# Kernel optimization log

Hardware: AMD Instinct MI355X
Metric: run time of the kernel (lower is better)

Reference implementation:

```python
import jax, jax.numpy as jnp
import numpy as np

B, S, D = 4, 2048, 1024
H, DK, DV = 16, 64, 64
NEG = -1e10


def setup_inputs() -> dict:
    key = jax.random.key(0)
    ks = jax.random.split(key, 7)
    queries = jax.random.normal(ks[0], (B, S, D), dtype=jnp.float32)
    keys = jax.random.normal(ks[1], (B, S, D), dtype=jnp.float32)
    values = jax.random.normal(ks[2], (B, S, D), dtype=jnp.float32)
    mask = jnp.ones((B, S, S), dtype=jnp.int32)
    # per-head Linear weights, torch layout [out, in]; stacked over heads
    Wq = jax.random.normal(ks[3], (H, DK, D), dtype=jnp.float32) / np.sqrt(D)
    Wk = jax.random.normal(ks[4], (H, DK, D), dtype=jnp.float32) / np.sqrt(D)
    Wv = jax.random.normal(ks[5], (H, DV, D), dtype=jnp.float32) / np.sqrt(D)
    Wo = jax.random.normal(ks[6], (D, H * DV), dtype=jnp.float32) / np.sqrt(H * DV)
    return {"queries": queries, "keys": keys, "values": values, "mask": mask,
            "Wq": Wq, "Wk": Wk, "Wv": Wv, "Wo": Wo}


def reference(queries, keys, values, mask, Wq, Wk, Wv, Wo):
    # per-head projections, vectorized over heads: y = x @ W_h^T
    q = jnp.einsum('bsd,hkd->bhsk', queries, Wq)   # [B,H,S,DK]
    k = jnp.einsum('btd,hkd->bhtk', keys, Wk)      # [B,H,S,DK]
    v = jnp.einsum('btd,hvd->bhtv', values, Wv)    # [B,H,S,DV]
    scores = jnp.einsum('bhsk,bhtk->bhst', q, k) / jnp.sqrt(jnp.asarray(DK, q.dtype))
    scores = jnp.where(mask[:, None, :, :] == 0, jnp.asarray(NEG, q.dtype), scores)
    attn = jax.nn.softmax(scores, axis=-1)
    out = jnp.einsum('bhst,bhtv->bhsv', attn, v)   # [B,H,S,DV]
    # torch.cat over heads on last dim == head-major concat per position
    out = out.transpose(0, 2, 1, 3).reshape(B, S, H * DV)
    return out @ Wo.T
```

## Files before the change

kernel.cpp:

```cpp
#include <hip/hip_runtime.h>
#include <stdint.h>

typedef __attribute__((ext_vector_type(4))) float f32x4;
typedef __attribute__((ext_vector_type(8))) __bf16 bf16x8;
typedef __attribute__((ext_vector_type(4))) __bf16 bf16x4;
typedef __attribute__((ext_vector_type(4))) short s16x4;
typedef __attribute__((ext_vector_type(2))) uint32_t u32x2;

#define MFMA16(a, b, c) __builtin_amdgcn_mfma_f32_16x16x32_bf16(a, b, c, 0, 0, 0)
#define MFMA16K16(a, b, c) __builtin_amdgcn_mfma_f32_16x16x16bf16_1k(a, b, c, 0, 0, 0)

#define B_ 4
#define S_ 2048
#define D_ 1024
#define H_ 16
#define NEG_ -1e10f
#define QSCALE 0.180336880f

__device__ __forceinline__ float ex2(float x) { return __builtin_amdgcn_exp2f(x); }

__device__ __forceinline__ void glds16(const void* gsrc, void* ldst) {
  __builtin_amdgcn_global_load_lds(
      (__attribute__((address_space(1))) void*)(gsrc),
      (__attribute__((address_space(3))) void*)(ldst),
      16, 0, 0);
}

__device__ __forceinline__ uint32_t pack_bf16(float a, float b) {
  uint32_t ua = (uint32_t)__builtin_bit_cast(unsigned short, (__bf16)a);
  uint32_t ub = (uint32_t)__builtin_bit_cast(unsigned short, (__bf16)b);
  return ua | (ub << 16);
}

__global__ __launch_bounds__(256) void prep(
    const float* __restrict__ xq, const float* __restrict__ xk, const float* __restrict__ xv,
    const float* __restrict__ wq, const float* __restrict__ wk, const float* __restrict__ wv,
    const float* __restrict__ wo,
    __bf16* __restrict__ oxq, __bf16* __restrict__ oxk, __bf16* __restrict__ oxv,
    __bf16* __restrict__ owq, __bf16* __restrict__ owk, __bf16* __restrict__ owv,
    __bf16* __restrict__ owo,
    const int* __restrict__ mask, uint32_t* __restrict__ bits, int* __restrict__ flags) {
  int bid = blockIdx.x, tid = threadIdx.x;
  __shared__ int andred;
  if (bid < 24576) {
    int z = bid >> 13, xb = bid & 8191;
    const float* in = (z == 0) ? xq : (z == 1) ? xk : xv;
    __bf16* out = (z == 0) ? oxq : (z == 1) ? oxk : oxv;
    int i = (xb * 256 + tid) * 4;
    float4 v = *(const float4*)(in + i);
    bf16x4 o;
    o.x = (__bf16)v.x; o.y = (__bf16)v.y; o.z = (__bf16)v.z; o.w = (__bf16)v.w;
    *(bf16x4*)(out + i) = o;
  } else if (bid < 28672) {
    int m = bid - 24576;
    int z = m >> 10, wb = m & 1023;
    const float* in = (z == 0) ? wq : (z == 1) ? wk : (z == 2) ? wv : wo;
    __bf16* out = (z == 0) ? owq : (z == 1) ? owk : (z == 2) ? owv : owo;
    int i = (wb * 256 + tid) * 4;
    float4 v = *(const float4*)(in + i);
    bf16x4 o;
    o.x = (__bf16)v.x; o.y = (__bf16)v.y; o.z = (__bf16)v.z; o.w = (__bf16)v.w;
    *(bf16x4*)(out + i) = o;
  } else {
    int m = bid - 28672;
    int tt = m & 15, st = (m >> 4) & 15, b = m >> 8;
    int w = tid >> 6, lane = tid & 63;
    if (tid == 0) andred = 1;
    __syncthreads();
    unsigned long long all1 = ~0ull;
    for (int rr = 0; rr < 32; rr++) {
      int srow = st * 128 + w * 32 + rr;
      #pragma unroll
      for (int half = 0; half < 2; half++) {
        int c = tt * 128 + half * 64 + lane;
        int mm = mask[((size_t)b * S_ + srow) * S_ + c];
        unsigned long long bal = __ballot(mm != 0);
        all1 &= bal;
        if (lane == 0) {
          uint32_t* dst = &bits[((size_t)b * S_ + srow) * 64 + tt * 4 + half * 2];
          dst[0] = (uint32_t)bal;
          dst[1] = (uint32_t)(bal >> 32);
        }
      }
    }
    if (all1 != ~0ull) atomicAnd(&andred, 0);
    __syncthreads();
    if (tid == 0) flags[(b * 16 + st) * 16 + tt] = andred;
  }
}

template <int MODE>
__global__ __launch_bounds__(256, 3) void gemm_bt(
    const __bf16* __restrict__ A0, const __bf16* __restrict__ A1, const __bf16* __restrict__ A2,
    const __bf16* __restrict__ W0, const __bf16* __restrict__ W1, const __bf16* __restrict__ W2,
    void* O0, void* O1, void* O2) {
  const int K = 1024;
  const __bf16* PA; const __bf16* PB; void* O;
  int pa_t, pb_t;
  if (MODE == 0) {
    if (blockIdx.z == 0)      { PA = W0; PB = A0; O = O0; pa_t = blockIdx.x; pb_t = blockIdx.y; }
    else if (blockIdx.z == 1) { PA = W1; PB = A1; O = O1; pa_t = blockIdx.x; pb_t = blockIdx.y; }
    else                      { PA = A2; PB = W2; O = O2; pa_t = blockIdx.y; pb_t = blockIdx.x; }
  } else { PA = W0; PB = A0; O = O0; pa_t = blockIdx.x; pb_t = blockIdx.y; }

  __shared__ __align__(16) __bf16 As[128 * 64];
  __shared__ __align__(16) __bf16 Bs[128 * 64];
  int tid = threadIdx.x, lane = tid & 63, w = tid >> 6;
  int wm = w >> 1, wn = w & 1;
  int g = lane >> 4, l15 = lane & 15;
  f32x4 acc[4][4] = {};
  const __bf16* Ablk = PA + (size_t)(pa_t * 128) * K;
  const __bf16* Bblk = PB + (size_t)(pb_t * 128) * K;

  for (int kt = 0; kt < K; kt += 64) {
    __syncthreads();
    #pragma unroll
    for (int r = 0; r < 4; r++) {
      int C = r * 256 + tid;
      int row = C >> 3, c = C & 7;
      int c0 = c ^ (row & 7);
      glds16(Ablk + (size_t)row * K + kt + c0 * 8, (char*)As + C * 16);
      glds16(Bblk + (size_t)row * K + kt + c0 * 8, (char*)Bs + C * 16);
    }
    __syncthreads();
    #pragma unroll
    for (int kkq = 0; kkq < 2; kkq++) {
      bf16x8 af[4], bfr[4];
      #pragma unroll
      for (int i = 0; i < 4; i++) {
        int row = wm * 64 + i * 16 + l15;
        int ch = (kkq * 4 + g) ^ (row & 7);
        af[i] = *(const bf16x8*)((const char*)As + row * 128 + ch * 16);
      }
      #pragma unroll
      for (int j = 0; j < 4; j++) {
        int row = wn * 64 + j * 16 + l15;
        int ch = (kkq * 4 + g) ^ (row & 7);
        bfr[j] = *(const bf16x8*)((const char*)Bs + row * 128 + ch * 16);
      }
      #pragma unroll
      for (int i = 0; i < 4; i++)
        #pragma unroll
        for (int j = 0; j < 4; j++)
          acc[i][j] = MFMA16(af[i], bfr[j], acc[i][j]);
    }
  }

  if (MODE == 1) {
    #pragma unroll
    for (int i = 0; i < 4; i++)
      #pragma unroll
      for (int j = 0; j < 4; j++) {
        int n0 = pa_t * 128 + wm * 64 + i * 16 + g * 4;
        int m = pb_t * 128 + wn * 64 + j * 16 + l15;
        *(f32x4*)((float*)O + (size_t)m * 1024 + n0) = acc[i][j];
      }
  } else if (blockIdx.z == 2) {
    #pragma unroll
    for (int i = 0; i < 4; i++)
      #pragma unroll
      for (int j = 0; j < 4; j++) {
        int s0 = pa_t * 128 + wm * 64 + i * 16 + g * 4;
        int dvg = pb_t * 128 + wn * 64 + j * 16 + l15;
        int b = s0 >> 11, s = s0 & 2047;
        int h = dvg >> 6, dv = dvg & 63;
        bf16x4 o;
        #pragma unroll
        for (int r = 0; r < 4; r++) o[r] = (__bf16)acc[i][j][r];
        *(bf16x4*)((__bf16*)O + (((size_t)b * 16 + h) * 64 + dv) * 2048 + s) = o;
      }
  } else {
    float scale = (blockIdx.z == 0) ? QSCALE : 1.0f;
    #pragma unroll
    for (int i = 0; i < 4; i++)
      #pragma unroll
      for (int j = 0; j < 4; j++) {
        int dkg = pa_t * 128 + wm * 64 + i * 16 + g * 4;
        int sg = pb_t * 128 + wn * 64 + j * 16 + l15;
        int h = dkg >> 6, dk = dkg & 63;
        int b = sg >> 11, s = sg & 2047;
        bf16x4 o;
        #pragma unroll
        for (int r = 0; r < 4; r++) o[r] = (__bf16)(acc[i][j][r] * scale);
        *(bf16x4*)((__bf16*)O + (((size_t)b * 16 + h) * 2048 + s) * 64 + dk) = o;
      }
  }
}

__global__ __launch_bounds__(256, 2) void attn(
    const __bf16* __restrict__ qp, const __bf16* __restrict__ kp,
    const __bf16* __restrict__ vt_, __bf16* __restrict__ aout,
    const uint32_t* __restrict__ bits, const int* __restrict__ flags) {
  int qt = blockIdx.x, bh = blockIdx.y, b = bh >> 4, h = bh & 15;
  int tid = threadIdx.x, lane = tid & 63, w = tid >> 6;
  int g = lane >> 4, l15 = lane & 15;

  __shared__ __align__(16) char smem[65536];

  const __bf16* Qg = qp + ((size_t)bh * S_ + qt * 128) * 64;
  const __bf16* Kg = kp + (size_t)bh * S_ * 64;
  const __bf16* Vg = vt_ + (size_t)bh * 64 * S_;

  #pragma unroll
  for (int r = 0; r < 4; r++) {
    int C = r * 256 + tid;
    int row = C >> 3, c = C & 7, c0 = c ^ (row & 7);
    glds16(Qg + row * 64 + c0 * 8, smem + C * 16);
  }
  __syncthreads();
  bf16x8 qf[2][2];
  #pragma unroll
  for (int i = 0; i < 2; i++)
    #pragma unroll
    for (int kkq = 0; kkq < 2; kkq++) {
      int row = w * 32 + i * 16 + l15;
      int ch = (kkq * 4 + g) ^ (row & 7);
      qf[i][kkq] = *(const bf16x8*)(smem + row * 128 + ch * 16);
    }
  __syncthreads();

  auto stageKV = [&](int kt2, int p) {
    char* Kl = smem + p * 32768;
    char* Vl = Kl + 16384;
    const __bf16* Ks = Kg + (size_t)kt2 * 128 * 64;
    #pragma unroll
    for (int r = 0; r < 4; r++) {
      int C = r * 256 + tid;
      int row = C >> 3, c = C & 7, c0 = c ^ (row & 7);
      glds16(Ks + row * 64 + c0 * 8, Kl + C * 16);
    }
    #pragma unroll
    for (int r = 0; r < 4; r++) {
      int C = r * 256 + tid;
      int row = C >> 4, c = C & 15;
      int c0 = (c & 8) | ((c & 7) ^ (row & 7));
      glds16(Vg + (size_t)row * S_ + kt2 * 128 + c0 * 8, Vl + C * 16);
    }
  };

  f32x4 oacc[4][2] = {};
  f32x4 sumacc[2] = {};
  float mst[2] = {-INFINITY, -INFINITY};
  const f32x4 zero4 = {0.f, 0.f, 0.f, 0.f};
  const s16x4 ones = {(short)0x3F80, (short)0x3F80, (short)0x3F80, (short)0x3F80};

  stageKV(0, 0);
  asm volatile("s_waitcnt vmcnt(0)" ::: "memory");
  __builtin_amdgcn_s_barrier();
  __builtin_amdgcn_sched_barrier(0);

  for (int kt = 0; kt < 16; kt++) {
    int cur = kt & 1;
    if (kt + 1 < 16) stageKV(kt + 1, cur ^ 1);
    __builtin_amdgcn_sched_barrier(0);

    const char* Klds = smem + cur * 32768;
    const char* Vlds = Klds + 16384;
    int fl = flags[(b * 16 + qt) * 16 + kt];

    f32x4 sacc[2][8];
    __builtin_amdgcn_s_setprio(1);
    #pragma unroll
    for (int jt = 0; jt < 8; jt++) {
      int row = jt * 16 + l15;
      bf16x8 kf0 = *(const bf16x8*)(Klds + row * 128 + (g ^ (row & 7)) * 16);
      bf16x8 kf1 = *(const bf16x8*)(Klds + row * 128 + ((4 + g) ^ (row & 7)) * 16);
      sacc[0][jt] = MFMA16(kf0, qf[0][0], zero4);
      sacc[0][jt] = MFMA16(kf1, qf[0][1], sacc[0][jt]);
      sacc[1][jt] = MFMA16(kf0, qf[1][0], zero4);
      sacc[1][jt] = MFMA16(kf1, qf[1][1], sacc[1][jt]);
    }
    __builtin_amdgcn_s_setprio(0);

    if (!fl) {
      #pragma unroll
      for (int i = 0; i < 2; i++) {
        int srow = qt * 128 + w * 32 + i * 16 + l15;
        const uint32_t* bw = &bits[((size_t)b * S_ + srow) * 64 + kt * 4];
        uint32_t mw[4] = {bw[0], bw[1], bw[2], bw[3]};
        #pragma unroll
        for (int jt = 0; jt < 8; jt++)
          #pragma unroll
          for (int r = 0; r < 4; r++) {
            int bitpos = (jt & 1) * 16 + g * 4 + r;
            if (!((mw[jt >> 1] >> bitpos) & 1)) sacc[i][jt][r] = NEG_;
          }
      }
    }

    float mx[2];
    #pragma unroll
    for (int i = 0; i < 2; i++) {
      float m = -INFINITY;
      #pragma unroll
      for (int jt = 0; jt < 8; jt++) {
        float a = fmaxf(fmaxf(sacc[i][jt][0], sacc[i][jt][1]),
                        fmaxf(sacc[i][jt][2], sacc[i][jt][3]));
        m = fmaxf(m, a);
      }
      m = fmaxf(m, __shfl_xor(m, 16));
      m = fmaxf(m, __shfl_xor(m, 32));
      mx[i] = m;
    }

    bool need = (mx[0] > mst[0] + 8.f) || (mx[1] > mst[1] + 8.f);
    if (__any(need)) {
      float alpha[2];
      #pragma unroll
      for (int i = 0; i < 2; i++) {
        float mnew = fmaxf(mst[i], mx[i]);
        alpha[i] = ex2(mst[i] - mnew);
        mst[i] = mnew;
      }
      #pragma unroll
      for (int vt = 0; vt < 4; vt++)
        #pragma unroll
        for (int i = 0; i < 2; i++)
          #pragma unroll
          for (int r = 0; r < 4; r++) oacc[vt][i][r] *= alpha[i];
      #pragma unroll
      for (int i = 0; i < 2; i++)
        #pragma unroll
        for (int r = 0; r < 4; r++) sumacc[i][r] *= alpha[i];
    }

    #pragma unroll
    for (int jt = 0; jt < 8; jt++) {
      s16x4 pf[2];
      #pragma unroll
      for (int i = 0; i < 2; i++) {
        float p0 = ex2(sacc[i][jt][0] - mst[i]);
        float p1 = ex2(sacc[i][jt][1] - mst[i]);
        float p2 = ex2(sacc[i][jt][2] - mst[i]);
        float p3 = ex2(sacc[i][jt][3] - mst[i]);
        u32x2 t;
        t.x = pack_bf16(p0, p1);
        t.y = pack_bf16(p2, p3);
        pf[i] = __builtin_bit_cast(s16x4, t);
      }
      int ch = jt * 2 + (g >> 1);
      __builtin_amdgcn_s_setprio(1);
      #pragma unroll
      for (int vt = 0; vt < 4; vt++) {
        int row = vt * 16 + l15;
        int chs = (ch & 8) | ((ch & 7) ^ (row & 7));
        s16x4 vv = *(const s16x4*)(Vlds + row * 256 + chs * 16 + (g & 1) * 8);
        oacc[vt][0] = MFMA16K16(vv, pf[0], oacc[vt][0]);
        oacc[vt][1] = MFMA16K16(vv, pf[1], oacc[vt][1]);
      }
      sumacc[0] = MFMA16K16(ones, pf[0], sumacc[0]);
      sumacc[1] = MFMA16K16(ones, pf[1], sumacc[1]);
      __builtin_amdgcn_s_setprio(0);
    }

    asm volatile("s_waitcnt vmcnt(0)" ::: "memory");
    __builtin_amdgcn_s_barrier();
    __builtin_amdgcn_sched_barrier(0);
  }

  #pragma unroll
  for (int i = 0; i < 2; i++) {
    float inv = 1.0f / sumacc[i][0];
    int srow = qt * 128 + w * 32 + i * 16 + l15;
    #pragma unroll
    for (int vt = 0; vt < 4; vt++) {
      bf16x4 o;
      #pragma unroll
      for (int r = 0; r < 4; r++) o[r] = (__bf16)(oacc[vt][i][r] * inv);
      *(bf16x4*)(aout + ((size_t)b * S_ + srow) * 1024 + h * 64 + vt * 16 + g * 4) = o;
    }
  }
}

extern "C" void kernel_launch(void* const* d_in, const int* in_sizes, int n_in,
                              void* d_out, int out_size, void* d_ws, size_t ws_size,
                              hipStream_t stream) {
  const float* queries = (const float*)d_in[0];
  const float* keys    = (const float*)d_in[1];
  const float* values  = (const float*)d_in[2];
  const int*   mask    = (const int*)d_in[3];
  const float* Wq      = (const float*)d_in[4];
  const float* Wk      = (const float*)d_in[5];
  const float* Wv      = (const float*)d_in[6];
  const float* Wo      = (const float*)d_in[7];

  char* ws = (char*)d_ws;
  __bf16* Xq  = (__bf16*)(ws + 0);
  __bf16* Xk  = (__bf16*)(ws + 16777216);
  __bf16* Xv  = (__bf16*)(ws + 33554432);
  __bf16* Wqb = (__bf16*)(ws + 50331648);
  __bf16* Wkb = (__bf16*)(ws + 52428800);
  __bf16* Wvb = (__bf16*)(ws + 54525952);
  __bf16* Wob = (__bf16*)(ws + 56623104);
  __bf16* qp  = (__bf16*)(ws + 58720256);
  __bf16* kp  = (__bf16*)(ws + 75497472);
  __bf16* vT  = (__bf16*)(ws + 92274688);
  uint32_t* bits = (uint32_t*)(ws + 109051904);
  int* flags     = (int*)(ws + 111149056);
  __bf16* aout = Xq;

  prep<<<29696, 256, 0, stream>>>(queries, keys, values, Wq, Wk, Wv, Wo,
                                  Xq, Xk, Xv, Wqb, Wkb, Wvb, Wob,
                                  mask, bits, flags);

  gemm_bt<0><<<dim3(8, 64, 3), 256, 0, stream>>>(Xq, Xk, Xv, Wqb, Wkb, Wvb,
                                                 (void*)qp, (void*)kp, (void*)vT);

  attn<<<dim3(16, 64), 256, 0, stream>>>(qp, kp, vT, aout, bits, flags);

  gemm_bt<1><<<dim3(8, 64, 1), 256, 0, stream>>>(aout, nullptr, nullptr, Wob, nullptr, nullptr,
                                                 (void*)d_out, nullptr, nullptr);
}
```

Baseline: 424.9 us.

## Swizzle block order and stage V through registers with half-swap to cut LDS conflicts

Remaps block indices in both the projection GEMM and the attention kernel so consecutive workgroups are spread across tiles, aiming for better cache locality across XCDs. The V tile is now loaded into registers and written to LDS with a row-dependent 8-byte half swap instead of a direct global-to-LDS copy. The matching read offset is XORed so the 8-byte V fragment reads hit fewer LDS bank conflicts. This adds register pressure and an explicit LDS write plus lgkmcnt wait at the end of each iteration, which can reduce the overlap of loads with compute.

```diff
diff --git a/kernel.cpp b/kernel.cpp
--- a/kernel.cpp
+++ b/kernel.cpp
@@ -95,13 +95,17 @@
     const __bf16* __restrict__ W0, const __bf16* __restrict__ W1, const __bf16* __restrict__ W2,
     void* O0, void* O1, void* O2) {
   const int K = 1024;
+  int lin = blockIdx.y * 8 + blockIdx.x;
+  int swz = (lin & 7) * 64 + (lin >> 3);
+  int bx = swz & 7, by = swz >> 3;
+
   const __bf16* PA; const __bf16* PB; void* O;
   int pa_t, pb_t;
   if (MODE == 0) {
-    if (blockIdx.z == 0)      { PA = W0; PB = A0; O = O0; pa_t = blockIdx.x; pb_t = blockIdx.y; }
-    else if (blockIdx.z == 1) { PA = W1; PB = A1; O = O1; pa_t = blockIdx.x; pb_t = blockIdx.y; }
-    else                      { PA = A2; PB = W2; O = O2; pa_t = blockIdx.y; pb_t = blockIdx.x; }
-  } else { PA = W0; PB = A0; O = O0; pa_t = blockIdx.x; pb_t = blockIdx.y; }
+    if (blockIdx.z == 0)      { PA = W0; PB = A0; O = O0; pa_t = bx; pb_t = by; }
+    else if (blockIdx.z == 1) { PA = W1; PB = A1; O = O1; pa_t = bx; pb_t = by; }
+    else                      { PA = A2; PB = W2; O = O2; pa_t = by; pb_t = bx; }
+  } else { PA = W0; PB = A0; O = O0; pa_t = bx; pb_t = by; }
 
   __shared__ __align__(16) __bf16 As[128 * 64];
   __shared__ __align__(16) __bf16 Bs[128 * 64];
@@ -191,9 +195,13 @@
     const __bf16* __restrict__ qp, const __bf16* __restrict__ kp,
     const __bf16* __restrict__ vt_, __bf16* __restrict__ aout,
     const uint32_t* __restrict__ bits, const int* __restrict__ flags) {
-  int qt = blockIdx.x, bh = blockIdx.y, b = bh >> 4, h = bh & 15;
+  int lin = blockIdx.y * 16 + blockIdx.x;
+  int swz = (lin & 7) * 128 + (lin >> 3);
+  int qt = swz & 15, bh = swz >> 4;
+  int b = bh >> 4, h = bh & 15;
   int tid = threadIdx.x, lane = tid & 63, w = tid >> 6;
   int g = lane >> 4, l15 = lane & 15;
+  int hs0 = ((g & 1) ^ ((l15 >> 3) & 1)) * 8;
 
   __shared__ __align__(16) char smem[65536];
 
@@ -219,22 +227,37 @@
     }
   __syncthreads();
 
-  auto stageKV = [&](int kt2, int p) {
+  auto stageK = [&](int kt2, int p) {
     char* Kl = smem + p * 32768;
-    char* Vl = Kl + 16384;
     const __bf16* Ks = Kg + (size_t)kt2 * 128 * 64;
     #pragma unroll
     for (int r = 0; r < 4; r++) {
       int C = r * 256 + tid;
       int row = C >> 3, c = C & 7, c0 = c ^ (row & 7);
-      glds16(Ks + row * 64 + c0 * 8, Kl + C * 16);
-    }
+      glds16(Ks + (size_t)row * 64 + c0 * 8, Kl + C * 16);
+    }
+  };
+  auto loadV = [&](int kt2, int4* vreg) {
     #pragma unroll
     for (int r = 0; r < 4; r++) {
       int C = r * 256 + tid;
       int row = C >> 4, c = C & 15;
       int c0 = (c & 8) | ((c & 7) ^ (row & 7));
-      glds16(Vg + (size_t)row * S_ + kt2 * 128 + c0 * 8, Vl + C * 16);
+      vreg[r] = *(const int4*)(Vg + (size_t)row * S_ + kt2 * 128 + c0 * 8);
+    }
+  };
+  auto writeV = [&](int p, const int4* vreg) {
+    char* Vl = smem + p * 32768 + 16384;
+    #pragma unroll
+    for (int r = 0; r < 4; r++) {
+      int C = r * 256 + tid;
+      int row = C >> 4;
+      int4 v = vreg[r];
+      bool sw = (row & 8) != 0;
+      int4 wv;
+      wv.x = sw ? v.z : v.x; wv.y = sw ? v.w : v.y;
+      wv.z = sw ? v.x : v.z; wv.w = sw ? v.y : v.w;
+      *(int4*)(Vl + C * 16) = wv;
     }
   };
 
@@ -244,14 +267,22 @@
   const f32x4 zero4 = {0.f, 0.f, 0.f, 0.f};
   const s16x4 ones = {(short)0x3F80, (short)0x3F80, (short)0x3F80, (short)0x3F80};
 
-  stageKV(0, 0);
+  int4 vreg[4];
+
+  stageK(0, 0);
+  loadV(0, vreg);
   asm volatile("s_waitcnt vmcnt(0)" ::: "memory");
+  writeV(0, vreg);
+  asm volatile("s_waitcnt lgkmcnt(0)" ::: "memory");
   __builtin_amdgcn_s_barrier();
   __builtin_amdgcn_sched_barrier(0);
 
   for (int kt = 0; kt < 16; kt++) {
     int cur = kt & 1;
-    if (kt + 1 < 16) stageKV(kt + 1, cur ^ 1);
+    if (kt + 1 < 16) {
+      stageK(kt + 1, cur ^ 1);
+      loadV(kt + 1, vreg);
+    }
     __builtin_amdgcn_sched_barrier(0);
 
     const char* Klds = smem + cur * 32768;
@@ -344,7 +375,7 @@
       for (int vt = 0; vt < 4; vt++) {
         int row = vt * 16 + l15;
         int chs = (ch & 8) | ((ch & 7) ^ (row & 7));
-        s16x4 vv = *(const s16x4*)(Vlds + row * 256 + chs * 16 + (g & 1) * 8);
+        s16x4 vv = *(const s16x4*)(Vlds + row * 256 + chs * 16 + hs0);
         oacc[vt][0] = MFMA16K16(vv, pf[0], oacc[vt][0]);
         oacc[vt][1] = MFMA16K16(vv, pf[1], oacc[vt][1]);
       }
@@ -354,6 +385,8 @@
     }
 
     asm volatile("s_waitcnt vmcnt(0)" ::: "memory");
+    if (kt + 1 < 16) writeV(cur ^ 1, vreg);
+    asm volatile("s_waitcnt lgkmcnt(0)" ::: "memory");
     __builtin_amdgcn_s_barrier();
     __builtin_amdgcn_sched_barrier(0);
   }
```

Result: slower. 433.5 us (+2.0%).
